# Kernel optimization log

Hardware: AMD Instinct MI355X
Metric: run time of the kernel (lower is better)

## Reference

```python
import jax, jax.numpy as jnp
import numpy as np

B, D, H, W = 8, 64, 128, 256
NH, NO = 64, 64  # nhidden, noutput


def _lstm_dir(x, Wih, Whh, bih, bhh, reverse=False):
    """Single-direction LSTM over x: [T, B, I] -> [T, B, H]. PyTorch gate order i,f,g,o."""
    if reverse:
        x = x[::-1]
    # Precompute input contribution to gates for all timesteps: [T, B, 4H]
    gx = jnp.einsum('tbi,gi->tbg', x, Wih) + (bih + bhh)
    Hd = Whh.shape[1]

    def step(carry, g):
        h, c = carry
        g = g + h @ Whh.T
        i, f, gg, o = jnp.split(g, 4, axis=-1)
        c = jax.nn.sigmoid(f) * c + jax.nn.sigmoid(i) * jnp.tanh(gg)
        h = jax.nn.sigmoid(o) * jnp.tanh(c)
        return (h, c), h

    Bt = x.shape[1]
    init = (jnp.zeros((Bt, Hd), x.dtype), jnp.zeros((Bt, Hd), x.dtype))
    _, hs = jax.lax.scan(step, init, gx)
    if reverse:
        hs = hs[::-1]
    return hs


def _bilstm(x, pf, pb):
    return jnp.concatenate(
        [_lstm_dir(x, *pf), _lstm_dir(x, *pb, reverse=True)], axis=-1)


def setup_inputs() -> dict:
    key = jax.random.key(0)
    ks = jax.random.split(key, 17)
    bound = 1.0 / np.sqrt(NH)

    def u(k_, shape):
        return jax.random.uniform(k_, shape, jnp.float32, -bound, bound)

    inp = {"img": jax.random.normal(ks[0], (B, D, H, W), jnp.float32)}
    # horizontal LSTM: input D -> hidden NH, bidirectional
    inp["h_Wih_f"] = u(ks[1], (4 * NH, D))
    inp["h_Whh_f"] = u(ks[2], (4 * NH, NH))
    inp["h_bih_f"] = u(ks[3], (4 * NH,))
    inp["h_bhh_f"] = u(ks[4], (4 * NH,))
    inp["h_Wih_b"] = u(ks[5], (4 * NH, D))
    inp["h_Whh_b"] = u(ks[6], (4 * NH, NH))
    inp["h_bih_b"] = u(ks[7], (4 * NH,))
    inp["h_bhh_b"] = u(ks[8], (4 * NH,))
    # vertical LSTM: input 2*NH -> hidden NO, bidirectional
    inp["v_Wih_f"] = u(ks[9], (4 * NO, 2 * NH))
    inp["v_Whh_f"] = u(ks[10], (4 * NO, NO))
    inp["v_bih_f"] = u(ks[11], (4 * NO,))
    inp["v_bhh_f"] = u(ks[12], (4 * NO,))
    inp["v_Wih_b"] = u(ks[13], (4 * NO, 2 * NH))
    inp["v_Whh_b"] = u(ks[14], (4 * NO, NO))
    inp["v_bih_b"] = u(ks[15], (4 * NO,))
    inp["v_bhh_b"] = u(ks[16], (4 * NO,))
    return inp


def reference(img,
              h_Wih_f, h_Whh_f, h_bih_f, h_bhh_f,
              h_Wih_b, h_Whh_b, h_bih_b, h_bhh_b,
              v_Wih_f, v_Whh_f, v_bih_f, v_bhh_f,
              v_Wih_b, v_Whh_b, v_bih_b, v_bhh_b):
    b, d, h, w = img.shape
    # BDHW -> WHBD -> [w, h*b, d]
    hin = jnp.transpose(img, (3, 2, 0, 1)).reshape(w, h * b, d)
    hout = _bilstm(hin,
                   (h_Wih_f, h_Whh_f, h_bih_f, h_bhh_f),
                   (h_Wih_b, h_Whh_b, h_bih_b, h_bhh_b))  # [w, h*b, 2*NH]
    # WHBD -> HWBD -> [h, w*b, 2*NH]
    vin = jnp.transpose(hout.reshape(w, h, b, -1), (1, 0, 2, 3)).reshape(h, w * b, -1)
    vout = _bilstm(vin,
                   (v_Wih_f, v_Whh_f, v_bih_f, v_bhh_f),
                   (v_Wih_b, v_Whh_b, v_bih_b, v_bhh_b))  # [h, w*b, 2*NO]
    # HWBD -> BDHW
    return jnp.transpose(vout.reshape(h, w, b, -1), (2, 3, 0, 1))
```

## Files before the change

kernel.cpp:

```cpp
#include <hip/hip_runtime.h>
#include <cstdint>


typedef _Float16 half8_t __attribute__((ext_vector_type(8)));
typedef float f32x4_t __attribute__((ext_vector_type(4)));

__device__ __forceinline__ float sigm(float x) {
    return __builtin_amdgcn_rcpf(1.0f + __builtin_amdgcn_exp2f(x * -1.44269504f));
}
__device__ __forceinline__ float tanh_(float x) {
    return 1.0f - 2.0f * __builtin_amdgcn_rcpf(1.0f + __builtin_amdgcn_exp2f(x * 2.88539008f));
}

__device__ __forceinline__ void block_sync() {
    asm volatile("s_waitcnt lgkmcnt(0)" ::: "memory");
    __builtin_amdgcn_s_barrier();
    asm volatile("" ::: "memory");
}

__device__ __forceinline__ half8_t load_w8(const float* p) {
    const float4 a = *(const float4*)p;
    const float4 b = *(const float4*)(p + 4);
    half8_t r;
    r[0] = (_Float16)a.x; r[1] = (_Float16)a.y; r[2] = (_Float16)a.z; r[3] = (_Float16)a.w;
    r[4] = (_Float16)b.x; r[5] = (_Float16)b.y; r[6] = (_Float16)b.z; r[7] = (_Float16)b.w;
    return r;
}

__device__ __forceinline__ void flush_chunk(const _Float16* bufCg, _Float16* hout,
                                            int hh0, int b, int dir, int wc0, int t)
{
    const int fm = t >> 5, fwi = (t >> 1) & 15, fhal = t & 1;
    const _Float16* src = bufCg + (fwi * 8 + fm) * 64 + fhal * 32;
    _Float16* dst = hout + ((size_t)(((hh0 + fm) * 8 + b) * 256 + wc0 + fwi) << 7)
                  + dir * 64 + fhal * 32;
    #pragma unroll
    for (int i = 0; i < 4; ++i)
        *(half8_t*)(dst + i * 8) = *(const half8_t*)(src + i * 8);
}

__device__ __forceinline__ void vflush(const float* Og, float* outp,
                                       int b, int dir, int w0, int hh0c, int t)
{
    const int ch = t & 63;
    const int hq = t >> 6;
    #pragma unroll
    for (int i = 0; i < 4; ++i) {
        const int hh = hq * 4 + i;
        float v[8];
        #pragma unroll
        for (int w = 0; w < 8; ++w) v[w] = Og[(hh * 8 + w) * 64 + ch];
        float4 a = make_float4(v[0], v[1], v[2], v[3]);
        float4 c = make_float4(v[4], v[5], v[6], v[7]);
        float* dst = outp + ((size_t)(b * 128 + dir * 64 + ch) * 128 + hh0c + hh) * 256 + w0;
        *(float4*)dst = a;
        *(float4*)(dst + 4) = c;
    }
}

__global__ __launch_bounds__(256) void k_xpose(const float* __restrict__ img, _Float16* __restrict__ xt)
{
    __shared__ float Ts[64 * 65];
    const int t  = threadIdx.x;
    const int wt = blockIdx.x & 3;
    const int hh = (blockIdx.x >> 2) & 127;
    const int b  = blockIdx.x >> 9;
    {
        const int d  = t >> 2;
        const int wq = (t & 3) * 16;
        const float* p = img + (((size_t)(b * 64 + d) * 128 + hh) * 256 + wt * 64 + wq);
        #pragma unroll
        for (int i = 0; i < 4; ++i) {
            const float4 v = *(const float4*)(p + i * 4);
            Ts[d * 65 + wq + i * 4 + 0] = v.x;
            Ts[d * 65 + wq + i * 4 + 1] = v.y;
            Ts[d * 65 + wq + i * 4 + 2] = v.z;
            Ts[d * 65 + wq + i * 4 + 3] = v.w;
        }
    }
    __syncthreads();
    const int wl = t >> 2;
    const int dq = (t & 3) * 16;
    half8_t o0, o1;
    #pragma unroll
    for (int i = 0; i < 8; ++i) o0[i] = (_Float16)Ts[(dq + i) * 65 + wl];
    #pragma unroll
    for (int i = 0; i < 8; ++i) o1[i] = (_Float16)Ts[(dq + 8 + i) * 65 + wl];
    _Float16* dst = xt + ((size_t)((b * 128 + hh) * 256 + wt * 64 + wl) << 6) + dq;
    *(half8_t*)(dst)     = o0;
    *(half8_t*)(dst + 8) = o1;
}

__global__ __launch_bounds__(256) void k_hrec(
    const _Float16* __restrict__ xt,
    const float* __restrict__ wihf, const float* __restrict__ whhf,
    const float* __restrict__ bif,  const float* __restrict__ bhf,
    const float* __restrict__ wihb, const float* __restrict__ whhb,
    const float* __restrict__ bib,  const float* __restrict__ bhb,
    _Float16* __restrict__ hout)
{
    __shared__ __align__(16) _Float16 Hbuf[2 * 1024];
    __shared__ __align__(16) _Float16 bufC[2 * 8192];
    const int t   = threadIdx.x;
    const int dir = blockIdx.x & 1;
    const int g   = blockIdx.x >> 1;
    const int b   = g & 7;
    const int hh0 = (g >> 3) * 8;
    const int wv  = t >> 6;
    const int l   = t & 63;
    const float* Wih = dir ? wihb : wihf;
    const float* Whh = dir ? whhb : whhf;
    const float* Bi  = dir ? bib  : bif;
    const float* Bh  = dir ? bhb  : bhf;

    half8_t Bf[4][4];
    float bias[4];
    #pragma unroll
    for (int p = 0; p < 4; ++p) {
        const int gate = p * 64 + wv * 16 + (l & 15);
        bias[p] = Bi[gate] + Bh[gate];
        #pragma unroll
        for (int kt = 0; kt < 4; ++kt) {
            const int k0 = kt * 32 + (l >> 4) * 8;
            const float* src = (kt < 2) ? (Wih + gate * 64 + k0) : (Whh + gate * 64 + (k0 - 64));
            Bf[p][kt] = load_w8(src);
        }
    }
    for (int i = t; i < 2048; i += 256) Hbuf[i] = (_Float16)0.0f;

    const int mrow = l & 7;
    const int ko   = l >> 4;
    const _Float16* xb = xt + (((size_t)(b * 128 + hh0 + mrow) * 256) << 6) + ko * 8;

    float c_[4] = {0.f, 0.f, 0.f, 0.f};
    const int col = l & 15;
    const int rq  = l >> 4;
    const int jg  = wv * 16 + col;
    const int hpos = (jg >> 5) * 512 + (((jg >> 3) & 3) * 16) * 8 + (jg & 7);

    auto wof = [&](int s) { int ss = s < 256 ? s : 255; return dir ? (255 - ss) : ss; };

    half8_t xE0 = *(const half8_t*)(xb + (wof(0) << 6));
    half8_t xE1 = *(const half8_t*)(xb + (wof(0) << 6) + 32);
    half8_t xO0 = *(const half8_t*)(xb + (wof(1) << 6));
    half8_t xO1 = *(const half8_t*)(xb + (wof(1) << 6) + 32);
    f32x4_t accx[4];
    #pragma unroll
    for (int p = 0; p < 4; ++p) {
        f32x4_t a = {bias[p], bias[p], bias[p], bias[p]};
        a = __builtin_amdgcn_mfma_f32_16x16x32_f16(xE0, Bf[p][0], a, 0, 0, 0);
        a = __builtin_amdgcn_mfma_f32_16x16x32_f16(xE1, Bf[p][1], a, 0, 0, 0);
        accx[p] = a;
    }
    xE0 = *(const half8_t*)(xb + (wof(2) << 6));
    xE1 = *(const half8_t*)(xb + (wof(2) << 6) + 32);
    __syncthreads();

    auto body = [&](int s, half8_t& xr0, half8_t& xr1) {
        const int grp = (s >> 4) & 1;
        if ((s & 15) == 0 && s > 0)
            flush_chunk(bufC + (grp ^ 1) * 8192, hout, hh0, b, dir,
                        dir ? (256 - s) : (s - 16), t);

        const int rdo = (s & 1) << 10;
        const half8_t H0 = *(const half8_t*)(Hbuf + rdo + l * 8);
        const half8_t H1 = *(const half8_t*)(Hbuf + rdo + 512 + l * 8);
        f32x4_t acc[4];
        #pragma unroll
        for (int p = 0; p < 4; ++p) {
            f32x4_t a = accx[p];
            a = __builtin_amdgcn_mfma_f32_16x16x32_f16(H0, Bf[p][2], a, 0, 0, 0);
            a = __builtin_amdgcn_mfma_f32_16x16x32_f16(H1, Bf[p][3], a, 0, 0, 0);
            acc[p] = a;
        }
        #pragma unroll
        for (int p = 0; p < 4; ++p) {
            f32x4_t a = {bias[p], bias[p], bias[p], bias[p]};
            a = __builtin_amdgcn_mfma_f32_16x16x32_f16(xr0, Bf[p][0], a, 0, 0, 0);
            a = __builtin_amdgcn_mfma_f32_16x16x32_f16(xr1, Bf[p][1], a, 0, 0, 0);
            accx[p] = a;
        }
        {
            const int wn = wof(s + 3);
            xr0 = *(const half8_t*)(xb + (wn << 6));
            xr1 = *(const half8_t*)(xb + (wn << 6) + 32);
        }
        float hv[4];
        #pragma unroll
        for (int r = 0; r < 4; ++r) {
            c_[r] = sigm(acc[1][r]) * c_[r] + sigm(acc[0][r]) * tanh_(acc[2][r]);
            hv[r] = sigm(acc[3][r]) * tanh_(c_[r]);
        }
        const int w   = wof(s);
        const int wro = ((s + 1) & 1) << 10;
        if (rq < 2) {
            #pragma unroll
            for (int r = 0; r < 4; ++r) {
                const int m = rq * 4 + r;
                Hbuf[wro + hpos + m * 8] = (_Float16)hv[r];
                bufC[grp * 8192 + ((w & 15) * 8 + m) * 64 + jg] = (_Float16)hv[r];
            }
        }
        block_sync();
    };

    for (int s2 = 0; s2 < 256; s2 += 2) {
        body(s2,     xO0, xO1);
        body(s2 + 1, xE0, xE1);
    }
    flush_chunk(bufC + 8192, hout, hh0, b, dir, dir ? 0 : 240, t);
}

__global__ __launch_bounds__(256) void k_vrec(
    const _Float16* __restrict__ hout,
    const float* __restrict__ wihf, const float* __restrict__ whhf,
    const float* __restrict__ bif,  const float* __restrict__ bhf,
    const float* __restrict__ wihb, const float* __restrict__ whhb,
    const float* __restrict__ bib,  const float* __restrict__ bhb,
    float* __restrict__ outp)
{
    __shared__ __align__(16) _Float16 Hbuf[2 * 1024];
    __shared__ __align__(16) float OutS[2 * 16 * 8 * 64];
    const int t   = threadIdx.x;
    const int dir = blockIdx.x & 1;
    const int g   = blockIdx.x >> 1;
    const int b   = g & 7;
    const int w0  = (g >> 3) * 8;
    const int wv  = t >> 6;
    const int l   = t & 63;
    const float* Wih = dir ? wihb : wihf;
    const float* Whh = dir ? whhb : whhf;
    const float* Bi  = dir ? bib  : bif;
    const float* Bh  = dir ? bhb  : bhf;

    half8_t Bf[4][6];
    float bias[4];
    #pragma unroll
    for (int p = 0; p < 4; ++p) {
        const int gate = p * 64 + wv * 16 + (l & 15);
        bias[p] = Bi[gate] + Bh[gate];
        #pragma unroll
        for (int kt = 0; kt < 6; ++kt) {
            const int k0 = kt * 32 + (l >> 4) * 8;
            const float* src = (kt < 4) ? (Wih + gate * 128 + k0) : (Whh + gate * 64 + (k0 - 128));
            Bf[p][kt] = load_w8(src);
        }
    }
    for (int i = t; i < 2048; i += 256) Hbuf[i] = (_Float16)0.0f;

    const int mrow = l & 7;
    const int ko   = l >> 4;
    const _Float16* xb = hout + ((size_t)(b * 256 + w0 + mrow) << 7) + ko * 8;

    float c_[4] = {0.f, 0.f, 0.f, 0.f};
    const int col = l & 15;
    const int rq  = l >> 4;
    const int jg  = wv * 16 + col;
    const int hpos = (jg >> 5) * 512 + (((jg >> 3) & 3) * 16) * 8 + (jg & 7);

    auto hof = [&](int s) { int ss = s < 128 ? s : 127; return dir ? (127 - ss) : ss; };

    half8_t xE[4], xO[4];
    #pragma unroll
    for (int kt = 0; kt < 4; ++kt) {
        xE[kt] = *(const half8_t*)(xb + ((size_t)hof(0) << 18) + kt * 32);
        xO[kt] = *(const half8_t*)(xb + ((size_t)hof(1) << 18) + kt * 32);
    }
    f32x4_t accx[4];
    #pragma unroll
    for (int p = 0; p < 4; ++p) {
        f32x4_t a = {bias[p], bias[p], bias[p], bias[p]};
        #pragma unroll
        for (int kt = 0; kt < 4; ++kt)
            a = __builtin_amdgcn_mfma_f32_16x16x32_f16(xE[kt], Bf[p][kt], a, 0, 0, 0);
        accx[p] = a;
    }
    #pragma unroll
    for (int kt = 0; kt < 4; ++kt)
        xE[kt] = *(const half8_t*)(xb + ((size_t)hof(2) << 18) + kt * 32);
    __syncthreads();

    auto body = [&](int s, half8_t (&xr)[4]) {
        const int grp = (s >> 4) & 1;
        if ((s & 15) == 0 && s > 0)
            vflush(OutS + (grp ^ 1) * 8192, outp, b, dir, w0,
                   dir ? (128 - s) : (s - 16), t);

        const int rdo = (s & 1) << 10;
        const half8_t H0 = *(const half8_t*)(Hbuf + rdo + l * 8);
        const half8_t H1 = *(const half8_t*)(Hbuf + rdo + 512 + l * 8);
        f32x4_t acc[4];
        #pragma unroll
        for (int p = 0; p < 4; ++p) {
            f32x4_t a = accx[p];
            a = __builtin_amdgcn_mfma_f32_16x16x32_f16(H0, Bf[p][4], a, 0, 0, 0);
            a = __builtin_amdgcn_mfma_f32_16x16x32_f16(H1, Bf[p][5], a, 0, 0, 0);
            acc[p] = a;
        }
        #pragma unroll
        for (int p = 0; p < 4; ++p) {
            f32x4_t a = {bias[p], bias[p], bias[p], bias[p]};
            #pragma unroll
            for (int kt = 0; kt < 4; ++kt)
                a = __builtin_amdgcn_mfma_f32_16x16x32_f16(xr[kt], Bf[p][kt], a, 0, 0, 0);
            accx[p] = a;
        }
        {
            const int hn = hof(s + 3);
            #pragma unroll
            for (int kt = 0; kt < 4; ++kt)
                xr[kt] = *(const half8_t*)(xb + ((size_t)hn << 18) + kt * 32);
        }
        float hv[4];
        #pragma unroll
        for (int r = 0; r < 4; ++r) {
            c_[r] = sigm(acc[1][r]) * c_[r] + sigm(acc[0][r]) * tanh_(acc[2][r]);
            hv[r] = sigm(acc[3][r]) * tanh_(c_[r]);
        }
        const int hh  = hof(s);
        const int wro = ((s + 1) & 1) << 10;
        if (rq < 2) {
            #pragma unroll
            for (int r = 0; r < 4; ++r) {
                const int m = rq * 4 + r;
                Hbuf[wro + hpos + m * 8] = (_Float16)hv[r];
                OutS[grp * 8192 + ((hh & 15) * 8 + m) * 64 + jg] = hv[r];
            }
        }
        block_sync();
    };

    for (int s2 = 0; s2 < 128; s2 += 2) {
        body(s2,     xO);
        body(s2 + 1, xE);
    }
    vflush(OutS + 8192, outp, b, dir, w0, dir ? 0 : 112, t);
}

extern "C" void kernel_launch(void* const* d_in, const int* in_sizes, int n_in,
                              void* d_out, int out_size, void* d_ws, size_t ws_size,
                              hipStream_t stream)
{
    const float* img   = (const float*)d_in[0];
    const float* hWihF = (const float*)d_in[1];
    const float* hWhhF = (const float*)d_in[2];
    const float* hBiF  = (const float*)d_in[3];
    const float* hBhF  = (const float*)d_in[4];
    const float* hWihB = (const float*)d_in[5];
    const float* hWhhB = (const float*)d_in[6];
    const float* hBiB  = (const float*)d_in[7];
    const float* hBhB  = (const float*)d_in[8];
    const float* vWihF = (const float*)d_in[9];
    const float* vWhhF = (const float*)d_in[10];
    const float* vBiF  = (const float*)d_in[11];
    const float* vBhF  = (const float*)d_in[12];
    const float* vWihB = (const float*)d_in[13];
    const float* vWhhB = (const float*)d_in[14];
    const float* vBiB  = (const float*)d_in[15];
    const float* vBhB  = (const float*)d_in[16];

    _Float16* XT   = (_Float16*)d_ws;
    _Float16* HOUT = (_Float16*)((char*)d_ws + (size_t)33554432);

    k_xpose<<<4096, 256, 0, stream>>>(img, XT);
    k_hrec<<<256, 256, 0, stream>>>(XT, hWihF, hWhhF, hBiF, hBhF,
                                    hWihB, hWhhB, hBiB, hBhB, HOUT);
    k_vrec<<<512, 256, 0, stream>>>(HOUT, vWihF, vWhhF, vBiF, vBhF,
                                    vWihB, vWhhB, vBiB, vBhB, (float*)d_out);

    (void)in_sizes; (void)n_in; (void)out_size; (void)ws_size;
}
```

Measured before the change: 522.1 us.

## Fill all 16 MFMA rows in vertical LSTM and spread hrec gate math across lanes

The vertical recurrence now packs 16 sequences (w positions) per block instead of 8, so every MFMA row carries real work and the grid halves to 256 blocks. Output staging and flushing are reorganised to cover 4 timesteps of 16 columns per flush. In the horizontal kernel, the idle upper-half lanes take over two of the four rows through cross-lane shuffles, so each lane evaluates the gate nonlinearities for 2 rows instead of 4. The trade is fewer blocks, which lowers parallelism across the device, plus added shuffle overhead and more frequent, smaller output flushes.

Result: faster. 452.6 us (-13.3%).

```diff
diff --git a/kernel.cpp b/kernel.cpp
--- a/kernel.cpp
+++ b/kernel.cpp
@@ -44,18 +44,13 @@
 {
     const int ch = t & 63;
     const int hq = t >> 6;
-    #pragma unroll
-    for (int i = 0; i < 4; ++i) {
-        const int hh = hq * 4 + i;
-        float v[8];
-        #pragma unroll
-        for (int w = 0; w < 8; ++w) v[w] = Og[(hh * 8 + w) * 64 + ch];
-        float4 a = make_float4(v[0], v[1], v[2], v[3]);
-        float4 c = make_float4(v[4], v[5], v[6], v[7]);
-        float* dst = outp + ((size_t)(b * 128 + dir * 64 + ch) * 128 + hh0c + hh) * 256 + w0;
-        *(float4*)dst = a;
-        *(float4*)(dst + 4) = c;
-    }
+    float v[16];
+    #pragma unroll
+    for (int w = 0; w < 16; ++w) v[w] = Og[hq * 1024 + w * 64 + ch];
+    float* dst = outp + ((size_t)(b * 128 + dir * 64 + ch) * 128 + hh0c + hq) * 256 + w0;
+    #pragma unroll
+    for (int i = 0; i < 4; ++i)
+        *(float4*)(dst + i * 4) = make_float4(v[i*4], v[i*4+1], v[i*4+2], v[i*4+3]);
 }
 
 __global__ __launch_bounds__(256) void k_xpose(const float* __restrict__ img, _Float16* __restrict__ xt)
@@ -132,11 +127,13 @@
     const int ko   = l >> 4;
     const _Float16* xb = xt + (((size_t)(b * 128 + hh0 + mrow) * 256) << 6) + ko * 8;
 
-    float c_[4] = {0.f, 0.f, 0.f, 0.f};
     const int col = l & 15;
     const int rq  = l >> 4;
     const int jg  = wv * 16 + col;
     const int hpos = (jg >> 5) * 512 + (((jg >> 3) & 3) * 16) * 8 + (jg & 7);
+    const int row0 = (rq >= 2) ? ((rq & 1) * 4 + 2) : (rq * 4);
+    const int row1 = row0 + 1;
+    float c2_[2] = {0.f, 0.f};
 
     auto wof = [&](int s) { int ss = s < 256 ? s : 255; return dir ? (255 - ss) : ss; };
 
@@ -185,28 +182,36 @@
             xr0 = *(const half8_t*)(xb + (wn << 6));
             xr1 = *(const half8_t*)(xb + (wn << 6) + 32);
         }
-        float hv[4];
-        #pragma unroll
-        for (int r = 0; r < 4; ++r) {
-            c_[r] = sigm(acc[1][r]) * c_[r] + sigm(acc[0][r]) * tanh_(acc[2][r]);
-            hv[r] = sigm(acc[3][r]) * tanh_(c_[r]);
-        }
+        float s2[4], s3[4];
+        #pragma unroll
+        for (int p = 0; p < 4; ++p) {
+            s2[p] = __shfl(acc[p][2], l & 31, 64);
+            s3[p] = __shfl(acc[p][3], l & 31, 64);
+        }
+        const bool hihalf = (rq >= 2);
+        float e0[4], e1[4];
+        #pragma unroll
+        for (int p = 0; p < 4; ++p) {
+            e0[p] = hihalf ? s2[p] : acc[p][0];
+            e1[p] = hihalf ? s3[p] : acc[p][1];
+        }
+        c2_[0] = sigm(e0[1]) * c2_[0] + sigm(e0[0]) * tanh_(e0[2]);
+        const float hv0 = sigm(e0[3]) * tanh_(c2_[0]);
+        c2_[1] = sigm(e1[1]) * c2_[1] + sigm(e1[0]) * tanh_(e1[2]);
+        const float hv1 = sigm(e1[3]) * tanh_(c2_[1]);
+
         const int w   = wof(s);
         const int wro = ((s + 1) & 1) << 10;
-        if (rq < 2) {
-            #pragma unroll
-            for (int r = 0; r < 4; ++r) {
-                const int m = rq * 4 + r;
-                Hbuf[wro + hpos + m * 8] = (_Float16)hv[r];
-                bufC[grp * 8192 + ((w & 15) * 8 + m) * 64 + jg] = (_Float16)hv[r];
-            }
-        }
+        Hbuf[wro + hpos + row0 * 8] = (_Float16)hv0;
+        Hbuf[wro + hpos + row1 * 8] = (_Float16)hv1;
+        bufC[grp * 8192 + ((w & 15) * 8 + row0) * 64 + jg] = (_Float16)hv0;
+        bufC[grp * 8192 + ((w & 15) * 8 + row1) * 64 + jg] = (_Float16)hv1;
         block_sync();
     };
 
-    for (int s2 = 0; s2 < 256; s2 += 2) {
-        body(s2,     xO0, xO1);
-        body(s2 + 1, xE0, xE1);
+    for (int s2i = 0; s2i < 256; s2i += 2) {
+        body(s2i,     xO0, xO1);
+        body(s2i + 1, xE0, xE1);
     }
     flush_chunk(bufC + 8192, hout, hh0, b, dir, dir ? 0 : 240, t);
 }
@@ -220,12 +225,12 @@
     float* __restrict__ outp)
 {
     __shared__ __align__(16) _Float16 Hbuf[2 * 1024];
-    __shared__ __align__(16) float OutS[2 * 16 * 8 * 64];
+    __shared__ __align__(16) float OutS[2 * 4 * 16 * 64];
     const int t   = threadIdx.x;
     const int dir = blockIdx.x & 1;
     const int g   = blockIdx.x >> 1;
     const int b   = g & 7;
-    const int w0  = (g >> 3) * 8;
+    const int w0  = (g >> 3) * 16;
     const int wv  = t >> 6;
     const int l   = t & 63;
     const float* Wih = dir ? wihb : wihf;
@@ -248,7 +253,7 @@
     }
     for (int i = t; i < 2048; i += 256) Hbuf[i] = (_Float16)0.0f;
 
-    const int mrow = l & 7;
+    const int mrow = l & 15;
     const int ko   = l >> 4;
     const _Float16* xb = hout + ((size_t)(b * 256 + w0 + mrow) << 7) + ko * 8;
 
@@ -281,10 +286,10 @@
     __syncthreads();
 
     auto body = [&](int s, half8_t (&xr)[4]) {
-        const int grp = (s >> 4) & 1;
-        if ((s & 15) == 0 && s > 0)
-            vflush(OutS + (grp ^ 1) * 8192, outp, b, dir, w0,
-                   dir ? (128 - s) : (s - 16), t);
+        const int grp = (s >> 2) & 1;
+        if ((s & 3) == 0 && s > 0)
+            vflush(OutS + (grp ^ 1) * 4096, outp, b, dir, w0,
+                   dir ? (128 - s) : (s - 4), t);
 
         const int rdo = (s & 1) << 10;
         const half8_t H0 = *(const half8_t*)(Hbuf + rdo + l * 8);
@@ -319,22 +324,20 @@
         }
         const int hh  = hof(s);
         const int wro = ((s + 1) & 1) << 10;
-        if (rq < 2) {
-            #pragma unroll
-            for (int r = 0; r < 4; ++r) {
-                const int m = rq * 4 + r;
-                Hbuf[wro + hpos + m * 8] = (_Float16)hv[r];
-                OutS[grp * 8192 + ((hh & 15) * 8 + m) * 64 + jg] = hv[r];
-            }
+        #pragma unroll
+        for (int r = 0; r < 4; ++r) {
+            const int m = rq * 4 + r;
+            Hbuf[wro + hpos + m * 8] = (_Float16)hv[r];
+            OutS[grp * 4096 + (hh & 3) * 1024 + m * 64 + jg] = hv[r];
         }
         block_sync();
     };
 
-    for (int s2 = 0; s2 < 128; s2 += 2) {
-        body(s2,     xO);
-        body(s2 + 1, xE);
-    }
-    vflush(OutS + 8192, outp, b, dir, w0, dir ? 0 : 112, t);
+    for (int s2i = 0; s2i < 128; s2i += 2) {
+        body(s2i,     xO);
+        body(s2i + 1, xE);
+    }
+    vflush(OutS + 4096, outp, b, dir, w0, dir ? 0 : 124, t);
 }
 
 extern "C" void kernel_launch(void* const* d_in, const int* in_sizes, int n_in,
@@ -365,7 +368,7 @@
     k_xpose<<<4096, 256, 0, stream>>>(img, XT);
     k_hrec<<<256, 256, 0, stream>>>(XT, hWihF, hWhhF, hBiF, hBhF,
                                     hWihB, hWhhB, hBiB, hBhB, HOUT);
-    k_vrec<<<512, 256, 0, stream>>>(HOUT, vWihF, vWhhF, vBiF, vBhF,
+    k_vrec<<<256, 256, 0, stream>>>(HOUT, vWihF, vWhhF, vBiF, vBhF,
                                     vWihB, vWhhB, vBiB, vBhB, (float*)d_out);
 
     (void)in_sizes; (void)n_in; (void)out_size; (void)ws_size;
```
